# Kernel tuning notes

Measured on AMD Instinct MI355X. Metric: run time of the kernel, lower is better.

The kernel has to match this reference:

```python
import jax, jax.numpy as jnp
import numpy as np

H, DK, DV, CHUNK = 4, 256, 256, 32
MIN_FLOOR, MAX_FLOOR, TEMP_MIN = 0.01, 0.1, 0.5


def _silu(x):
    return x * jax.nn.sigmoid(x)


def _causal_dw_conv(x_bcl, w_ck):
    # depthwise causal 1-D conv: x (b, C, L), w (C, K)
    K = w_ck.shape[-1]
    return jax.lax.conv_general_dilated(
        x_bcl, w_ck[:, None, :], window_strides=(1,), padding=[(K - 1, 0)],
        feature_group_count=x_bcl.shape[1])


def _l2norm(x):
    return x * jax.lax.rsqrt(jnp.sum(x * x, axis=-1, keepdims=True) + 1e-6)


def _delta_rule_chunkwise(q, k, v, beta, chunk=CHUNK):
    # q,k: (b,h,L,dk)  v: (b,h,L,dv)  beta: (b,h,L); L divisible by chunk
    b, h, L, dk = q.shape
    dv = v.shape[-1]
    n = L // chunk
    q = _l2norm(q)
    k = _l2norm(k)
    v = v * beta[..., None]
    kb = k * beta[..., None]
    qc, kc, vc, kbc = (t.reshape(b, h, n, chunk, -1) for t in (q, k, v, kb))
    # in-chunk inverse: the torch row loop computes (I + tril(k_beta k^T, -1))^{-1}
    A = jnp.einsum('bhncd,bhned->bhnce', kbc, kc)
    eye = jnp.eye(chunk, dtype=q.dtype)
    T = eye + jnp.tril(A, -1)
    inv = jax.scipy.linalg.solve_triangular(
        T, jnp.broadcast_to(eye, T.shape), lower=True, unit_diagonal=True)
    u = inv @ vc      # (b,h,n,c,dv)
    w = inv @ kbc     # (b,h,n,c,dk)
    strict = jnp.triu(jnp.ones((chunk, chunk), dtype=bool), 1)

    def step(S, xs):
        q_i, k_i, u_i, w_i = xs
        att = jnp.where(strict, 0.0, jnp.einsum('bhcd,bhed->bhce', q_i, k_i))
        u_adj = u_i - jnp.einsum('bhck,bhkd->bhcd', w_i, S)
        o = jnp.einsum('bhck,bhkd->bhcd', q_i, S) + att @ u_adj
        S = S + jnp.einsum('bhck,bhcd->bhkd', k_i, u_adj)
        return S, o

    mv = lambda t: jnp.moveaxis(t, 2, 0)  # chunks to scan axis
    S0 = jnp.zeros((b, h, dk, dv), dtype=q.dtype)
    S, outs = jax.lax.scan(step, S0, (mv(qc), mv(kc), mv(u), mv(w)))
    out = jnp.moveaxis(outs, 0, 2).reshape(b, h, L, dv)
    return out, S


def _fir(x, filt):
    # x: (b,l,h,d), filt: (h,d,K) depthwise causal FIR per (head, channel)
    b, l, h, d = x.shape
    xc = x.transpose(0, 2, 3, 1).reshape(b, h * d, l)
    y = _causal_dw_conv(xc, filt.reshape(h * d, -1))
    return y.reshape(b, h, d, l).transpose(0, 3, 1, 2)


def setup_inputs() -> dict:
    key = jax.random.key(0)
    ks = iter(jax.random.split(key, 32))
    B, L, D = 4, 2048, 1024
    kd, vd = H * DK, H * DV
    rn = lambda shp, s=0.02: jax.random.normal(next(ks), shp, jnp.float32) * s
    fir = lambda K: (jnp.zeros((H, DV, K), jnp.float32).at[..., -1].set(1.0)
                     + 0.01 * jax.random.normal(next(ks), (H, DV, K), jnp.float32))
    return dict(
        hidden_states=jax.random.normal(next(ks), (B, L, D), jnp.float32),
        Wq=rn((D, kd)), Wk=rn((D, kd)), Wv=rn((D, vd)),
        q_conv_w=rn((kd, 4), 0.3), k_conv_w=rn((kd, 4), 0.3), v_conv_w=rn((vd, 4), 0.3),
        Wb=rn((D, H)),
        fir_w3=fir(3), fir_w7=fir(7), fir_w15=fir(15), fir_w31=fir(31),
        router_W1=rn((D + DV * H * 5, 2 * D)), router_b1=jnp.zeros((2 * D,), jnp.float32),
        router_W2=rn((2 * D, H * 5)), router_b2=jnp.zeros((H * 5,), jnp.float32),
        id_gate_W=rn((D, H)), id_gate_b=jnp.full((H,), 2.0, jnp.float32),
        log_tau=jnp.zeros((H,), jnp.float32),
        o_norm_w=jnp.ones((DV,), jnp.float32),
        Wo=rn((vd, D)))


def reference(hidden_states, Wq, Wk, Wv, q_conv_w, k_conv_w, v_conv_w, Wb,
              fir_w3, fir_w7, fir_w15, fir_w31,
              router_W1, router_b1, router_W2, router_b2,
              id_gate_W, id_gate_b, log_tau, o_norm_w, Wo):
    B, L, D = hidden_states.shape
    conv = lambda x, w: _silu(_causal_dw_conv(x.transpose(0, 2, 1), w)).transpose(0, 2, 1)
    q = conv(hidden_states @ Wq, q_conv_w).reshape(B, L, H, DK)
    k = conv(hidden_states @ Wk, k_conv_w).reshape(B, L, H, DK)
    v_direct = conv(hidden_states @ Wv, v_conv_w).reshape(B, L, H, DV)
    beta = jax.nn.sigmoid(hidden_states @ Wb)  # (B,L,H)
    delta_out, _ = _delta_rule_chunkwise(
        q.transpose(0, 2, 1, 3), k.transpose(0, 2, 1, 3),
        v_direct.transpose(0, 2, 1, 3), beta.transpose(0, 2, 1))
    delta_out = delta_out.transpose(0, 2, 1, 3)  # (B,L,H,DV)
    paths = [_fir(v_direct, f) for f in (fir_w3, fir_w7, fir_w15, fir_w31)] + [delta_out]
    # token-adaptive value/context split
    p_value = jax.nn.sigmoid(hidden_states @ id_gate_W + id_gate_b)  # (B,L,H)
    floor_tok = MIN_FLOOR + (MAX_FLOOR - MIN_FLOOR) * (1.0 - p_value)
    p_value_adj = (1.0 - floor_tok) * p_value
    context_mass = 1.0 - p_value_adj
    # router over [hidden, all context paths]
    router_in = jnp.concatenate(
        [hidden_states] + [p.reshape(B, L, H * DV) for p in paths], axis=-1)
    hmid = jax.nn.gelu(router_in @ router_W1 + router_b1, approximate=False)
    logits = (hmid @ router_W2 + router_b2).reshape(B, L, H, 5)
    tau = jnp.maximum(jnp.exp(log_tau), TEMP_MIN)  # (H,)
    probs = jax.nn.softmax(logits / tau[:, None], axis=-1)
    ctx = sum(probs[..., i:i + 1] * paths[i] for i in range(5))
    o = context_mass[..., None] * ctx + p_value_adj[..., None] * v_direct
    # per-head RMSNorm then output projection
    o = o * jax.lax.rsqrt(jnp.mean(o * o, axis=-1, keepdims=True) + 1e-5) * o_norm_w
    return o.reshape(B, L, H * DV) @ Wo
```

## Files before the change

### kernel.cpp

```cpp
#include <hip/hip_runtime.h>
#include <math.h>

#define NTOK   8192
#define LSEQ   2048
#define NCHUNK 64

typedef short bhalf8 __attribute__((ext_vector_type(8)));
typedef float floatx4 __attribute__((ext_vector_type(4)));

__device__ inline ushort f2bf(float f) {
  uint u = __float_as_uint(f);
  u += 0x7FFFu + ((u >> 16) & 1u);
  return (ushort)(u >> 16);
}
__device__ inline float bf2f(ushort h) {
  return __uint_as_float(((uint)h) << 16);
}

#define GLD_LDS16(g, s) __builtin_amdgcn_global_load_lds(                      \
    (const __attribute__((address_space(1))) void*)(g),                        \
    (__attribute__((address_space(3))) void*)(s), 16, 0, 0)

__global__ __launch_bounds__(256)
void cvt_bf16(const float* __restrict__ x, ushort* __restrict__ y, int n8) {
  int i = blockIdx.x * 256 + threadIdx.x;
  if (i >= n8) return;
  const float4* xp = (const float4*)x;
  float4 a = xp[2 * i], b = xp[2 * i + 1];
  uint4 o;
  o.x = (uint)f2bf(a.x) | ((uint)f2bf(a.y) << 16);
  o.y = (uint)f2bf(a.z) | ((uint)f2bf(a.w) << 16);
  o.z = (uint)f2bf(b.x) | ((uint)f2bf(b.y) << 16);
  o.w = (uint)f2bf(b.z) | ((uint)f2bf(b.w) << 16);
  ((uint4*)y)[i] = o;
}

__global__ __launch_bounds__(256)
void cvt_t(const float* __restrict__ x, ushort* __restrict__ y, int R, int C) {
  __shared__ float tile[32][33];
  int r0 = blockIdx.y * 32, c0 = blockIdx.x * 32;
  int tr = threadIdx.x >> 5;
  int tc = threadIdx.x & 31;
  #pragma unroll
  for (int rr = tr; rr < 32; rr += 8)
    tile[rr][tc] = x[(size_t)(r0 + rr) * C + c0 + tc];
  __syncthreads();
  #pragma unroll
  for (int rr = tr; rr < 32; rr += 8)
    y[(size_t)(c0 + rr) * R + r0 + tc] = f2bf(tile[tc][rr]);
}

template<int ACC>
__global__ __launch_bounds__(256)
void gemm_bf(const ushort* __restrict__ A, const ushort* __restrict__ BT,
             float* __restrict__ C, int K, int lda, int ldbt, int ldc) {
  __shared__ ushort Asm[128 * 32];
  __shared__ ushort Bsm[128 * 32];
  const int t = threadIdx.x;
  const int w = t >> 6, l = t & 63;
  const int m0 = blockIdx.y * 128, n0 = blockIdx.x * 128;
  const int wr = w >> 1, wc = w & 1;
  const int srow = l >> 2;
  const int scol = (l & 3) * 8;
  const int fr = l & 15;
  const int fk = (l >> 4) * 8;

  floatx4 acc[4][4];
  #pragma unroll
  for (int i = 0; i < 4; i++)
    #pragma unroll
    for (int j = 0; j < 4; j++)
      #pragma unroll
      for (int r = 0; r < 4; r++) acc[i][j][r] = 0.f;

  for (int k0 = 0; k0 < K; k0 += 32) {
    __syncthreads();
    #pragma unroll
    for (int j = 0; j < 2; j++) {
      int row = w * 32 + j * 16 + srow;
      GLD_LDS16(A + (size_t)(m0 + row) * lda + k0 + scol,
                Asm + (w * 32 + j * 16) * 32);
      GLD_LDS16(BT + (size_t)(n0 + row) * ldbt + k0 + scol,
                Bsm + (w * 32 + j * 16) * 32);
    }
    __syncthreads();
    bhalf8 af[4], bf_[4];
    #pragma unroll
    for (int i = 0; i < 4; i++)
      af[i] = *(const bhalf8*)&Asm[(wr * 64 + i * 16 + fr) * 32 + fk];
    #pragma unroll
    for (int j = 0; j < 4; j++)
      bf_[j] = *(const bhalf8*)&Bsm[(wc * 64 + j * 16 + fr) * 32 + fk];
    #pragma unroll
    for (int i = 0; i < 4; i++)
      #pragma unroll
      for (int j = 0; j < 4; j++)
        acc[i][j] = __builtin_amdgcn_mfma_f32_16x16x32_bf16(af[i], bf_[j],
                                                            acc[i][j], 0, 0, 0);
  }
  const int crow = (l >> 4) * 4;
  const int ccol = l & 15;
  #pragma unroll
  for (int i = 0; i < 4; i++)
    #pragma unroll
    for (int j = 0; j < 4; j++) {
      float* cp = &C[(size_t)(m0 + wr * 64 + i * 16 + crow) * ldc +
                     n0 + wc * 64 + j * 16 + ccol];
      #pragma unroll
      for (int r = 0; r < 4; r++) {
        if (ACC) cp[(size_t)r * ldc] += acc[i][j][r];
        else     cp[(size_t)r * ldc]  = acc[i][j][r];
      }
    }
}

struct APtrs { const ushort* p[6]; };

__global__ __launch_bounds__(256)
void gemm_router(APtrs ap, const ushort* __restrict__ BT,
                 float* __restrict__ C) {
  __shared__ ushort Asm[128 * 32];
  __shared__ ushort Bsm[128 * 32];
  const int t = threadIdx.x;
  const int w = t >> 6, l = t & 63;
  const int m0 = blockIdx.y * 128, n0 = blockIdx.x * 128;
  const int wr = w >> 1, wc = w & 1;
  const int srow = l >> 2;
  const int scol = (l & 3) * 8;
  const int fr = l & 15;
  const int fk = (l >> 4) * 8;

  floatx4 acc[4][4];
  #pragma unroll
  for (int i = 0; i < 4; i++)
    #pragma unroll
    for (int j = 0; j < 4; j++)
      #pragma unroll
      for (int r = 0; r < 4; r++) acc[i][j][r] = 0.f;

  for (int k0 = 0; k0 < 6144; k0 += 32) {
    const ushort* Abase = ap.p[k0 >> 10];
    const int kk = k0 & 1023;
    __syncthreads();
    #pragma unroll
    for (int j = 0; j < 2; j++) {
      int row = w * 32 + j * 16 + srow;
      GLD_LDS16(Abase + (size_t)(m0 + row) * 1024 + kk + scol,
                Asm + (w * 32 + j * 16) * 32);
      GLD_LDS16(BT + (size_t)(n0 + row) * 6144 + k0 + scol,
                Bsm + (w * 32 + j * 16) * 32);
    }
    __syncthreads();
    bhalf8 af[4], bf_[4];
    #pragma unroll
    for (int i = 0; i < 4; i++)
      af[i] = *(const bhalf8*)&Asm[(wr * 64 + i * 16 + fr) * 32 + fk];
    #pragma unroll
    for (int j = 0; j < 4; j++)
      bf_[j] = *(const bhalf8*)&Bsm[(wc * 64 + j * 16 + fr) * 32 + fk];
    #pragma unroll
    for (int i = 0; i < 4; i++)
      #pragma unroll
      for (int j = 0; j < 4; j++)
        acc[i][j] = __builtin_amdgcn_mfma_f32_16x16x32_bf16(af[i], bf_[j],
                                                            acc[i][j], 0, 0, 0);
  }
  const int crow = (l >> 4) * 4;
  const int ccol = l & 15;
  #pragma unroll
  for (int i = 0; i < 4; i++)
    #pragma unroll
    for (int j = 0; j < 4; j++) {
      float* cp = &C[(size_t)(m0 + wr * 64 + i * 16 + crow) * 1024 +
                     n0 + wc * 64 + j * 16 + ccol];
      #pragma unroll
      for (int r = 0; r < 4; r++) cp[(size_t)r * 1024] = acc[i][j][r];
    }
}

__global__ __launch_bounds__(256)
void conv4_silu(const float* __restrict__ x, const float* __restrict__ w,
                float* __restrict__ y) {
  int idx = blockIdx.x * 256 + threadIdx.x;
  int c = idx & 1023;
  int bl = idx >> 10;
  int l = bl & (LSEQ - 1);
  float w0 = w[c * 4 + 0], w1 = w[c * 4 + 1], w2 = w[c * 4 + 2], w3 = w[c * 4 + 3];
  float acc = x[idx] * w3;
  if (l >= 1) acc += x[idx - 1024] * w2;
  if (l >= 2) acc += x[idx - 2048] * w1;
  if (l >= 3) acc += x[idx - 3072] * w0;
  y[idx] = acc / (1.f + expf(-acc));
}

__global__ __launch_bounds__(256)
void pack_fir(const float* __restrict__ f3w, const float* __restrict__ f7w,
              const float* __restrict__ f15w, const float* __restrict__ f31w,
              float* __restrict__ fwTp) {
  int i = blockIdx.x * 256 + threadIdx.x;
  if (i >= 57344) return;
  int row = i >> 10, c = i & 1023;
  float val;
  if (row < 3)       val = f3w[c * 3 + row];
  else if (row < 10) val = f7w[c * 7 + (row - 3)];
  else if (row < 25) val = f15w[c * 15 + (row - 10)];
  else               val = f31w[c * 31 + (row - 25)];
  fwTp[i] = val;
}

__global__ __launch_bounds__(256)
void fir_all(const float* __restrict__ v, const float* __restrict__ fwTp,
             ushort* __restrict__ y3, ushort* __restrict__ y7,
             ushort* __restrict__ y15, ushort* __restrict__ y31) {
  int idx = blockIdx.x * 256 + threadIdx.x;
  int c = idx & 1023;
  int l = (idx >> 10) & (LSEQ - 1);
  float a3 = 0.f, a7 = 0.f, a15 = 0.f, a31 = 0.f;
  #pragma unroll
  for (int back = 30; back >= 0; back--) {
    float x = (l >= back) ? v[idx - back * 1024] : 0.f;
    a31 += x * fwTp[(25 + 30 - back) * 1024 + c];
    if (back <= 14) a15 += x * fwTp[(10 + 14 - back) * 1024 + c];
    if (back <= 6)  a7  += x * fwTp[(3 + 6 - back) * 1024 + c];
    if (back <= 2)  a3  += x * fwTp[(2 - back) * 1024 + c];
  }
  y3[idx]  = f2bf(a3);
  y7[idx]  = f2bf(a7);
  y15[idx] = f2bf(a15);
  y31[idx] = f2bf(a31);
}

__global__ __launch_bounds__(256)
void beta_pv(const float* __restrict__ hs, const float* __restrict__ Wb,
             const float* __restrict__ idW, const float* __restrict__ idb,
             float* __restrict__ beta, float* __restrict__ pv) {
  int tok = blockIdx.x;
  int h = threadIdx.x >> 6;
  int lane = threadIdx.x & 63;
  const float* hrow = hs + (size_t)tok * 1024;
  float s1 = 0.f, s2 = 0.f;
  #pragma unroll
  for (int j = 0; j < 16; j++) {
    int d = lane + j * 64;
    float hv = hrow[d];
    s1 += hv * Wb[d * 4 + h];
    s2 += hv * idW[d * 4 + h];
  }
  #pragma unroll
  for (int off = 32; off; off >>= 1) {
    s1 += __shfl_down(s1, off);
    s2 += __shfl_down(s2, off);
  }
  if (lane == 0) {
    beta[tok * 4 + h] = 1.f / (1.f + expf(-s1));
    pv[tok * 4 + h] = 1.f / (1.f + expf(-(s2 + idb[h])));
  }
}

__global__ __launch_bounds__(256)
void l2norm_qk(float* __restrict__ q, float* __restrict__ k) {
  int tok = blockIdx.x;
  int h = threadIdx.x >> 6;
  int lane = threadIdx.x & 63;
  size_t base = (size_t)tok * 1024 + h * 256 + lane * 4;
  {
    float4* p = (float4*)(q + base);
    float4 v = *p;
    float ss = v.x * v.x + v.y * v.y + v.z * v.z + v.w * v.w;
    #pragma unroll
    for (int off = 32; off; off >>= 1) ss += __shfl_xor(ss, off);
    float sc = rsqrtf(ss + 1e-6f);
    v.x *= sc; v.y *= sc; v.z *= sc; v.w *= sc;
    *p = v;
  }
  {
    float4* p = (float4*)(k + base);
    float4 v = *p;
    float ss = v.x * v.x + v.y * v.y + v.z * v.z + v.w * v.w;
    #pragma unroll
    for (int off = 32; off; off >>= 1) ss += __shfl_xor(ss, off);
    float sc = rsqrtf(ss + 1e-6f);
    v.x *= sc; v.y *= sc; v.z *= sc; v.w *= sc;
    *p = v;
  }
}

__global__ __launch_bounds__(256)
void chunk_prep(const float* __restrict__ q, const float* __restrict__ k,
                const float* __restrict__ v, const float* __restrict__ beta,
                ushort* __restrict__ attf, float* __restrict__ ub,
                ushort* __restrict__ wfb, ushort* __restrict__ qfb,
                ushort* __restrict__ ktb) {
  __shared__ float kbuf[32 * 260];
  __shared__ float qbuf[32 * 260];
  __shared__ float Am[32 * 32];
  __shared__ float bet[32];
  const int t = threadIdx.x;
  const int blk = blockIdx.x;
  const int n = blk & 63, bh = blk >> 6;
  const int h = bh & 3, b = bh >> 2;
  const size_t rowbase = (size_t)b * LSEQ + n * 32;
  const int cbase = h * 256;
  const int srow = t >> 6, scol = (t & 63) * 4;
  const size_t fb = (size_t)blk * 8192;

  #pragma unroll
  for (int rep = 0; rep < 8; rep++) {
    int r = rep * 4 + srow;
    *(float4*)&kbuf[r * 260 + scol] =
        *(const float4*)&k[(rowbase + r) * 1024 + cbase + scol];
    *(float4*)&qbuf[r * 260 + scol] =
        *(const float4*)&q[(rowbase + r) * 1024 + cbase + scol];
  }
  if (t < 32) bet[t] = beta[(rowbase + t) * 4 + h];
  __syncthreads();

  #pragma unroll
  for (int e = 0; e < 4; e++) {
    int idx = t + e * 256;
    int i = idx >> 5, jc = idx & 31;
    float da = 0.f, dq = 0.f;
    for (int d0 = 0; d0 < 256; d0 += 4) {
      float4 kj = *(float4*)&kbuf[jc * 260 + d0];
      float4 ki = *(float4*)&kbuf[i * 260 + d0];
      float4 qi = *(float4*)&qbuf[i * 260 + d0];
      da += ki.x * kj.x + ki.y * kj.y + ki.z * kj.z + ki.w * kj.w;
      dq += qi.x * kj.x + qi.y * kj.y + qi.z * kj.z + qi.w * kj.w;
    }
    Am[i * 32 + jc] = (jc < i) ? bet[i] * da : 0.f;
    float av = (jc <= i) ? dq : 0.f;
    attf[(size_t)blk * 1024 + (i >> 4) * 512 +
         ((i & 15) + ((jc >> 3) & 3) * 16) * 8 + (jc & 7)] = f2bf(av);
  }
  __syncthreads();

  #pragma unroll
  for (int cg = 0; cg < 4; cg++) {
    bhalf8 pk;
    #pragma unroll
    for (int j = 0; j < 8; j++)
      pk[j] = (short)f2bf(kbuf[(cg * 8 + j) * 260 + t]);
    *(bhalf8*)&ktb[fb + (t >> 4) * 512 + ((t & 15) + cg * 16) * 8] = pk;
  }

  #pragma unroll 1
  for (int i = 0; i < 32; i++) {
    float val = bet[i] * kbuf[i * 260 + t];
    for (int j = 0; j < i; j++) val -= Am[i * 32 + j] * kbuf[j * 260 + t];
    kbuf[i * 260 + t] = val;
  }
  __syncthreads();

  #pragma unroll
  for (int rep = 0; rep < 4; rep++) {
    int p = rep * 256 + t;
    int c = p & 31, dk8 = p >> 5;
    size_t pos = fb + ((size_t)(dk8 >> 2) * 2 + (c >> 4)) * 512 +
                 ((c & 15) + (dk8 & 3) * 16) * 8;
    bhalf8 pw, pq;
    #pragma unroll
    for (int j = 0; j < 8; j++) {
      pw[j] = (short)f2bf(kbuf[c * 260 + dk8 * 8 + j]);
      pq[j] = (short)f2bf(qbuf[c * 260 + dk8 * 8 + j]);
    }
    *(bhalf8*)&wfb[pos] = pw;
    *(bhalf8*)&qfb[pos] = pq;
  }
  __syncthreads();

  #pragma unroll
  for (int rep = 0; rep < 8; rep++) {
    int r = rep * 4 + srow;
    *(float4*)&qbuf[r * 260 + scol] =
        *(const float4*)&v[(rowbase + r) * 1024 + cbase + scol];
  }
  __syncthreads();
  #pragma unroll 1
  for (int i = 0; i < 32; i++) {
    float val = bet[i] * qbuf[i * 260 + t];
    for (int j = 0; j < i; j++) val -= Am[i * 32 + j] * qbuf[j * 260 + t];
    qbuf[i * 260 + t] = val;
  }
  for (int j = 0; j < 32; j++)
    ub[(rowbase + j) * 1024 + cbase + t] = qbuf[j * 260 + t];
}

__global__ __launch_bounds__(256)
void delta_scan(const ushort* __restrict__ wfb, const ushort* __restrict__ qfb,
                const ushort* __restrict__ ktb, const ushort* __restrict__ attf,
                const float* __restrict__ ub, ushort* __restrict__ outb) {
  __shared__ ushort wS[8192];
  __shared__ ushort qS[8192];
  __shared__ ushort kTS[8192];
  __shared__ ushort attS[1024];
  __shared__ ushort SbT[16 * 264];
  __shared__ ushort uaT[16 * 40];
  __shared__ float pbufW[4 * 544];
  __shared__ float pbufQ[4 * 544];
  __shared__ float oacc[544];
  const int t = threadIdx.x;
  const int w = t >> 6, l = t & 63;
  const int col16 = l & 15, g = l >> 4;
  const int blk = blockIdx.x;
  const int dsl = blk & 15, bh = blk >> 4;
  const int h = bh & 3, b = bh >> 2;
  const int dbase = h * 256 + dsl * 16;

  floatx4 S_acc[4];
  #pragma unroll
  for (int m = 0; m < 4; m++)
    #pragma unroll
    for (int r = 0; r < 4; r++) S_acc[m][r] = 0.f;

  for (int n = 0; n < NCHUNK; n++) {
    const size_t cb = ((size_t)(bh * 64 + n)) * 8192;
    const size_t ab = ((size_t)(bh * 64 + n)) * 1024;
    const size_t rowbase = (size_t)b * LSEQ + n * 32;

    #pragma unroll
    for (int m = 0; m < 4; m++) {
      uint lo = (uint)f2bf(S_acc[m][0]) | ((uint)f2bf(S_acc[m][1]) << 16);
      uint hi = (uint)f2bf(S_acc[m][2]) | ((uint)f2bf(S_acc[m][3]) << 16);
      uint2 pk; pk.x = lo; pk.y = hi;
      *(uint2*)&SbT[col16 * 264 + w * 64 + m * 16 + g * 4] = pk;
    }
    #pragma unroll
    for (int i = 0; i < 4; i++) {
      GLD_LDS16(wfb + cb + (w * 4 + i) * 512 + l * 8, &wS[(w * 4 + i) * 512]);
      GLD_LDS16(qfb + cb + (w * 4 + i) * 512 + l * 8, &qS[(w * 4 + i) * 512]);
      GLD_LDS16(ktb + cb + (w * 4 + i) * 512 + l * 8, &kTS[(w * 4 + i) * 512]);
    }
    if (w == 2) {
      GLD_LDS16(attf + ab + l * 8, &attS[0]);
      GLD_LDS16(attf + ab + 512 + l * 8, &attS[512]);
    }
    float u0 = ub[(rowbase + (t >> 4)) * 1024 + dbase + (t & 15)];
    float u1 = ub[(rowbase + 16 + (t >> 4)) * 1024 + dbase + (t & 15)];
    __syncthreads();

    floatx4 pw0, pw1, pq0, pq1;
    #pragma unroll
    for (int r = 0; r < 4; r++) { pw0[r] = 0.f; pw1[r] = 0.f; pq0[r] = 0.f; pq1[r] = 0.f; }
    #pragma unroll
    for (int s = 0; s < 2; s++) {
      const int koff = w * 2 + s;
      bhalf8 sb = *(const bhalf8*)&SbT[col16 * 264 + koff * 32 + g * 8];
      bhalf8 wa0 = *(const bhalf8*)&wS[((koff * 2 + 0) * 64 + l) * 8];
      bhalf8 wa1 = *(const bhalf8*)&wS[((koff * 2 + 1) * 64 + l) * 8];
      bhalf8 qa0 = *(const bhalf8*)&qS[((koff * 2 + 0) * 64 + l) * 8];
      bhalf8 qa1 = *(const bhalf8*)&qS[((koff * 2 + 1) * 64 + l) * 8];
      pw0 = __builtin_amdgcn_mfma_f32_16x16x32_bf16(wa0, sb, pw0, 0, 0, 0);
      pw1 = __builtin_amdgcn_mfma_f32_16x16x32_bf16(wa1, sb, pw1, 0, 0, 0);
      pq0 = __builtin_amdgcn_mfma_f32_16x16x32_bf16(qa0, sb, pq0, 0, 0, 0);
      pq1 = __builtin_amdgcn_mfma_f32_16x16x32_bf16(qa1, sb, pq1, 0, 0, 0);
    }
    #pragma unroll
    for (int r = 0; r < 4; r++) {
      pbufW[w * 544 + (g * 4 + r) * 17 + col16] = pw0[r];
      pbufW[w * 544 + (16 + g * 4 + r) * 17 + col16] = pw1[r];
      pbufQ[w * 544 + (g * 4 + r) * 17 + col16] = pq0[r];
      pbufQ[w * 544 + (16 + g * 4 + r) * 17 + col16] = pq1[r];
    }
    __syncthreads();

    {
      const int row = t >> 4, c2 = t & 15;
      const int i0 = row * 17 + c2, i1 = (row + 16) * 17 + c2;
      float wsA = pbufW[i0] + pbufW[544 + i0] + pbufW[1088 + i0] + pbufW[1632 + i0];
      float wsB = pbufW[i1] + pbufW[544 + i1] + pbufW[1088 + i1] + pbufW[1632 + i1];
      float qsA = pbufQ[i0] + pbufQ[544 + i0] + pbufQ[1088 + i0] + pbufQ[1632 + i0];
      float qsB = pbufQ[i1] + pbufQ[544 + i1] + pbufQ[1088 + i1] + pbufQ[1632 + i1];
      oacc[i0] = qsA;
      oacc[i1] = qsB;
      uaT[c2 * 40 + row] = f2bf(u0 - wsA);
      uaT[c2 * 40 + row + 16] = f2bf(u1 - wsB);
    }
    __syncthreads();

    bhalf8 uB = *(const bhalf8*)&uaT[col16 * 40 + g * 8];
    #pragma unroll
    for (int m = 0; m < 4; m++) {
      bhalf8 ka = *(const bhalf8*)&kTS[((w * 4 + m) * 64 + l) * 8];
      S_acc[m] = __builtin_amdgcn_mfma_f32_16x16x32_bf16(ka, uB, S_acc[m], 0, 0, 0);
    }
    if (w < 2) {
      floatx4 z;
      #pragma unroll
      for (int r = 0; r < 4; r++) z[r] = 0.f;
      bhalf8 aa = *(const bhalf8*)&attS[(w * 64 + l) * 8];
      floatx4 oat = __builtin_amdgcn_mfma_f32_16x16x32_bf16(aa, uB, z, 0, 0, 0);
      #pragma unroll
      for (int r = 0; r < 4; r++) {
        int row = w * 16 + g * 4 + r;
        float ov = oacc[row * 17 + col16] + oat[r];
        outb[(rowbase + row) * 1024 + dbase + col16] = f2bf(ov);
      }
    }
    __syncthreads();
  }
}

__global__ __launch_bounds__(256)
void gelu_bias(float* __restrict__ x, const float* __restrict__ bias) {
  int idx = blockIdx.x * 256 + threadIdx.x;
  float4* p = (float4*)x + idx;
  float4 v = *p;
  int col = (idx * 4) & 1023;
  float4 bb = *(const float4*)&bias[col];
  float xs[4] = {v.x + bb.x, v.y + bb.y, v.z + bb.z, v.w + bb.w};
  #pragma unroll
  for (int j = 0; j < 4; j++)
    xs[j] = 0.5f * xs[j] * (1.f + erff(xs[j] * 0.70710678118654752f));
  v.x = xs[0]; v.y = xs[1]; v.z = xs[2]; v.w = xs[3];
  *p = v;
}

template<int FIRST>
__global__ __launch_bounds__(256)
void logits_acc(const float* __restrict__ hmid, const float* __restrict__ W2,
                const float* __restrict__ b2, float* __restrict__ logits) {
  __shared__ float hrow[1024];
  __shared__ float part[8][20];
  int tok = blockIdx.x, t = threadIdx.x;
  ((float4*)hrow)[t] = ((const float4*)(hmid + (size_t)tok * 1024))[t];
  __syncthreads();
  if (t < 160) {
    int col = t % 20, seg = t / 20;
    float acc = 0.f;
    for (int kk = 0; kk < 128; kk++) {
      int k2 = seg * 128 + kk;
      acc += hrow[k2] * W2[(size_t)k2 * 20 + col];
    }
    part[seg][col] = acc;
  }
  __syncthreads();
  if (t < 20) {
    float s = 0.f;
    #pragma unroll
    for (int g = 0; g < 8; g++) s += part[g][t];
    if (FIRST) logits[(size_t)tok * 20 + t] = b2[t] + s;
    else       logits[(size_t)tok * 20 + t] += s;
  }
}

__global__ __launch_bounds__(256)
void softmax_probs(const float* __restrict__ logits, const float* __restrict__ ltau,
                   float* __restrict__ probs) {
  int idx = blockIdx.x * 256 + threadIdx.x;
  int tok = idx >> 2, h = idx & 3;
  float tau = expf(ltau[h]);
  tau = tau < 0.5f ? 0.5f : tau;
  float x[5]; float m = -1e30f;
  #pragma unroll
  for (int i = 0; i < 5; i++) {
    x[i] = logits[(size_t)tok * 20 + h * 5 + i] / tau;
    m = fmaxf(m, x[i]);
  }
  float s = 0.f;
  #pragma unroll
  for (int i = 0; i < 5; i++) { x[i] = expf(x[i] - m); s += x[i]; }
  float inv = 1.f / s;
  #pragma unroll
  for (int i = 0; i < 5; i++) probs[(size_t)tok * 20 + h * 5 + i] = x[i] * inv;
}

__global__ __launch_bounds__(256)
void mix_rms(const ushort* __restrict__ f3, const ushort* __restrict__ f7,
             const ushort* __restrict__ f15, const ushort* __restrict__ f31,
             const ushort* __restrict__ dlt, const float* __restrict__ v,
             const float* __restrict__ probs, const float* __restrict__ pv,
             const float* __restrict__ onw, ushort* __restrict__ omix) {
  int tok = blockIdx.x;
  int h = threadIdx.x >> 6;
  int lane = threadIdx.x & 63;
  size_t base = (size_t)tok * 1024 + h * 256 + lane * 4;
  const float* pp = probs + (size_t)tok * 20 + h * 5;
  float p0 = pp[0], p1 = pp[1], p2 = pp[2], p3 = pp[3], p4 = pp[4];
  float pvv = pv[tok * 4 + h];
  float floor_tok = 0.01f + 0.09f * (1.f - pvv);
  float pa = (1.f - floor_tok) * pvv;
  float cm = 1.f - pa;
  ushort4 a4 = *(const ushort4*)&f3[base];
  ushort4 b4 = *(const ushort4*)&f7[base];
  ushort4 c4 = *(const ushort4*)&f15[base];
  ushort4 d4 = *(const ushort4*)&f31[base];
  ushort4 e4 = *(const ushort4*)&dlt[base];
  float4 vv = *(const float4*)&v[base];
  float av[4] = {bf2f(a4.x), bf2f(a4.y), bf2f(a4.z), bf2f(a4.w)};
  float bv[4] = {bf2f(b4.x), bf2f(b4.y), bf2f(b4.z), bf2f(b4.w)};
  float cv[4] = {bf2f(c4.x), bf2f(c4.y), bf2f(c4.z), bf2f(c4.w)};
  float dv[4] = {bf2f(d4.x), bf2f(d4.y), bf2f(d4.z), bf2f(d4.w)};
  float ev[4] = {bf2f(e4.x), bf2f(e4.y), bf2f(e4.z), bf2f(e4.w)};
  float vvv[4] = {vv.x, vv.y, vv.z, vv.w};
  float o[4];
  #pragma unroll
  for (int j = 0; j < 4; j++)
    o[j] = cm * (p0 * av[j] + p1 * bv[j] + p2 * cv[j] + p3 * dv[j] + p4 * ev[j]) +
           pa * vvv[j];
  float ss = o[0]*o[0] + o[1]*o[1] + o[2]*o[2] + o[3]*o[3];
  #pragma unroll
  for (int off = 32; off; off >>= 1) ss += __shfl_xor(ss, off);
  float sc = rsqrtf(ss * (1.f / 256.f) + 1e-5f);
  float4 wn = *(const float4*)&onw[lane * 4];
  ushort4 res;
  res.x = f2bf(o[0] * sc * wn.x); res.y = f2bf(o[1] * sc * wn.y);
  res.z = f2bf(o[2] * sc * wn.z); res.w = f2bf(o[3] * sc * wn.w);
  *(ushort4*)&omix[base] = res;
}

extern "C" void kernel_launch(void* const* d_in, const int* in_sizes, int n_in,
                              void* d_out, int out_size, void* d_ws, size_t ws_size,
                              hipStream_t stream) {
  const float* hs  = (const float*)d_in[0];
  const float* Wq  = (const float*)d_in[1];
  const float* Wk  = (const float*)d_in[2];
  const float* Wv  = (const float*)d_in[3];
  const float* qcw = (const float*)d_in[4];
  const float* kcw = (const float*)d_in[5];
  const float* vcw = (const float*)d_in[6];
  const float* Wb  = (const float*)d_in[7];
  const float* f3w = (const float*)d_in[8];
  const float* f7w = (const float*)d_in[9];
  const float* f15w= (const float*)d_in[10];
  const float* f31w= (const float*)d_in[11];
  const float* rW1 = (const float*)d_in[12];
  const float* rb1 = (const float*)d_in[13];
  const float* rW2 = (const float*)d_in[14];
  const float* rb2 = (const float*)d_in[15];
  const float* igW = (const float*)d_in[16];
  const float* igb = (const float*)d_in[17];
  const float* ltau= (const float*)d_in[18];
  const float* onw = (const float*)d_in[19];
  const float* Wo  = (const float*)d_in[20];
  float* out = (float*)d_out;
  float* ws  = (float*)d_ws;

  float* pre    = ws;
  float* qb     = ws +  8388608;
  float* kb     = ws + 16777216;
  float* vb     = ws + 25165824;
  float* ub     = ws + 33554432;
  float* wbuf   = ws + 41943040;
  float* dlt    = ws + 50331648;
  float* fwTp   = ws + 58720256;
  float* beta   = ws + 59768832;
  float* pv     = ws + 59801600;
  float* logits = ws + 59834368;
  float* probs  = ws + 59998208;

  ushort* hs_bf1 = (ushort*)ub;
  ushort* WqT    = (ushort*)(ub + 4194304);
  ushort* WkT    = WqT + 1048576;
  ushort* WvT    = WkT + 1048576;
  ushort* ktb    = (ushort*)pre;
  ushort* attfb  = (ushort*)(pre + 4194304);
  ushort* wfb    = (ushort*)wbuf;
  ushort* qfb    = (ushort*)(wbuf + 4194304);
  ushort* f3b    = (ushort*)ub;
  ushort* f7b    = (ushort*)(ub + 4194304);
  ushort* f15b   = (ushort*)wbuf;
  ushort* f31b   = (ushort*)(wbuf + 4194304);
  ushort* dltb   = (ushort*)dlt;
  ushort* omixb  = (ushort*)(dlt + 4194304);
  ushort* hs_bf2 = (ushort*)kb;
  ushort* WoT    = (ushort*)(kb + 4194304);
  ushort* W1T    = (ushort*)qb;
  float*  hmid   = pre;

  dim3 blk(256);
  dim3 gg(8, 64);

  cvt_bf16<<<4096, blk, 0, stream>>>(hs, hs_bf1, 1048576);
  cvt_t<<<dim3(32, 32), blk, 0, stream>>>(Wq, WqT, 1024, 1024);
  cvt_t<<<dim3(32, 32), blk, 0, stream>>>(Wk, WkT, 1024, 1024);
  cvt_t<<<dim3(32, 32), blk, 0, stream>>>(Wv, WvT, 1024, 1024);
  gemm_bf<0><<<gg, blk, 0, stream>>>(hs_bf1, WqT, pre, 1024, 1024, 1024, 1024);
  conv4_silu<<<32768, blk, 0, stream>>>(pre, qcw, qb);
  gemm_bf<0><<<gg, blk, 0, stream>>>(hs_bf1, WkT, pre, 1024, 1024, 1024, 1024);
  conv4_silu<<<32768, blk, 0, stream>>>(pre, kcw, kb);
  gemm_bf<0><<<gg, blk, 0, stream>>>(hs_bf1, WvT, pre, 1024, 1024, 1024, 1024);
  conv4_silu<<<32768, blk, 0, stream>>>(pre, vcw, vb);

  beta_pv<<<8192, blk, 0, stream>>>(hs, Wb, igW, igb, beta, pv);
  l2norm_qk<<<8192, blk, 0, stream>>>(qb, kb);

  chunk_prep<<<1024, blk, 0, stream>>>(qb, kb, vb, beta, attfb, ub, wfb, qfb, ktb);
  delta_scan<<<256, blk, 0, stream>>>(wfb, qfb, ktb, attfb, ub, dltb);

  pack_fir<<<224, blk, 0, stream>>>(f3w, f7w, f15w, f31w, fwTp);
  fir_all<<<32768, blk, 0, stream>>>(vb, fwTp, f3b, f7b, f15b, f31b);

  cvt_bf16<<<4096, blk, 0, stream>>>(hs, hs_bf2, 1048576);
  cvt_t<<<dim3(64, 192), blk, 0, stream>>>(rW1, W1T, 6144, 2048);
  cvt_t<<<dim3(32, 32), blk, 0, stream>>>(Wo, WoT, 1024, 1024);

  APtrs ap;
  ap.p[0] = hs_bf2; ap.p[1] = f3b; ap.p[2] = f7b;
  ap.p[3] = f15b;   ap.p[4] = f31b; ap.p[5] = dltb;
  for (int nh = 0; nh < 2; nh++) {
    gemm_router<<<gg, blk, 0, stream>>>(ap, W1T + (size_t)nh * 1024 * 6144, hmid);
    gelu_bias<<<8192, blk, 0, stream>>>(hmid, rb1 + nh * 1024);
    if (nh == 0) logits_acc<1><<<8192, blk, 0, stream>>>(hmid, rW2, rb2, logits);
    else         logits_acc<0><<<8192, blk, 0, stream>>>(hmid, rW2 + (size_t)1024 * 20, rb2, logits);
  }
  softmax_probs<<<128, blk, 0, stream>>>(logits, ltau, probs);

  mix_rms<<<8192, blk, 0, stream>>>(f3b, f7b, f15b, f31b, dltb, vb, probs, pv,
                                    onw, omixb);
  gemm_bf<0><<<gg, blk, 0, stream>>>(omixb, WoT, out, 1024, 1024, 1024, 1024);
}
```

Baseline: 1.247 ms.

## Store GEMM tiles in MFMA fragment order and fuse bias+GELU into router GEMM

Changes the LDS staging layout of both GEMM kernels so each 16-row subtile is written in the exact lane order the MFMA fragment reads, making fragment loads contiguous and removing LDS bank conflicts. Also fuses the router's first-layer bias add and exact GELU into the router GEMM epilogue, eliminating the standalone gelu_bias kernel and its read/write pass over the hidden buffer. The epilogue now does erff per output element inside the GEMM, adding some register and ALU pressure there.

```diff
diff --git a/kernel.cpp b/kernel.cpp
--- a/kernel.cpp
+++ b/kernel.cpp
@@ -60,10 +60,8 @@
   const int w = t >> 6, l = t & 63;
   const int m0 = blockIdx.y * 128, n0 = blockIdx.x * 128;
   const int wr = w >> 1, wc = w & 1;
-  const int srow = l >> 2;
-  const int scol = (l & 3) * 8;
-  const int fr = l & 15;
-  const int fk = (l >> 4) * 8;
+  const int frow = l & 15;
+  const int fcol = (l >> 4) * 8;
 
   floatx4 acc[4][4];
   #pragma unroll
@@ -77,20 +75,19 @@
     __syncthreads();
     #pragma unroll
     for (int j = 0; j < 2; j++) {
-      int row = w * 32 + j * 16 + srow;
-      GLD_LDS16(A + (size_t)(m0 + row) * lda + k0 + scol,
-                Asm + (w * 32 + j * 16) * 32);
-      GLD_LDS16(BT + (size_t)(n0 + row) * ldbt + k0 + scol,
-                Bsm + (w * 32 + j * 16) * 32);
+      int sub = w * 2 + j;
+      int row = sub * 16 + frow;
+      GLD_LDS16(A + (size_t)(m0 + row) * lda + k0 + fcol, Asm + sub * 512);
+      GLD_LDS16(BT + (size_t)(n0 + row) * ldbt + k0 + fcol, Bsm + sub * 512);
     }
     __syncthreads();
     bhalf8 af[4], bf_[4];
     #pragma unroll
     for (int i = 0; i < 4; i++)
-      af[i] = *(const bhalf8*)&Asm[(wr * 64 + i * 16 + fr) * 32 + fk];
+      af[i] = *(const bhalf8*)&Asm[(wr * 4 + i) * 512 + l * 8];
     #pragma unroll
     for (int j = 0; j < 4; j++)
-      bf_[j] = *(const bhalf8*)&Bsm[(wc * 64 + j * 16 + fr) * 32 + fk];
+      bf_[j] = *(const bhalf8*)&Bsm[(wc * 4 + j) * 512 + l * 8];
     #pragma unroll
     for (int i = 0; i < 4; i++)
       #pragma unroll
@@ -118,17 +115,15 @@
 
 __global__ __launch_bounds__(256)
 void gemm_router(APtrs ap, const ushort* __restrict__ BT,
-                 float* __restrict__ C) {
+                 const float* __restrict__ bias, float* __restrict__ C) {
   __shared__ ushort Asm[128 * 32];
   __shared__ ushort Bsm[128 * 32];
   const int t = threadIdx.x;
   const int w = t >> 6, l = t & 63;
   const int m0 = blockIdx.y * 128, n0 = blockIdx.x * 128;
   const int wr = w >> 1, wc = w & 1;
-  const int srow = l >> 2;
-  const int scol = (l & 3) * 8;
-  const int fr = l & 15;
-  const int fk = (l >> 4) * 8;
+  const int frow = l & 15;
+  const int fcol = (l >> 4) * 8;
 
   floatx4 acc[4][4];
   #pragma unroll
@@ -144,20 +139,19 @@
     __syncthreads();
     #pragma unroll
     for (int j = 0; j < 2; j++) {
-      int row = w * 32 + j * 16 + srow;
-      GLD_LDS16(Abase + (size_t)(m0 + row) * 1024 + kk + scol,
-                Asm + (w * 32 + j * 16) * 32);
-      GLD_LDS16(BT + (size_t)(n0 + row) * 6144 + k0 + scol,
-                Bsm + (w * 32 + j * 16) * 32);
+      int sub = w * 2 + j;
+      int row = sub * 16 + frow;
+      GLD_LDS16(Abase + (size_t)(m0 + row) * 1024 + kk + fcol, Asm + sub * 512);
+      GLD_LDS16(BT + (size_t)(n0 + row) * 6144 + k0 + fcol, Bsm + sub * 512);
     }
     __syncthreads();
     bhalf8 af[4], bf_[4];
     #pragma unroll
     for (int i = 0; i < 4; i++)
-      af[i] = *(const bhalf8*)&Asm[(wr * 64 + i * 16 + fr) * 32 + fk];
+      af[i] = *(const bhalf8*)&Asm[(wr * 4 + i) * 512 + l * 8];
     #pragma unroll
     for (int j = 0; j < 4; j++)
-      bf_[j] = *(const bhalf8*)&Bsm[(wc * 64 + j * 16 + fr) * 32 + fk];
+      bf_[j] = *(const bhalf8*)&Bsm[(wc * 4 + j) * 512 + l * 8];
     #pragma unroll
     for (int i = 0; i < 4; i++)
       #pragma unroll
@@ -171,10 +165,14 @@
   for (int i = 0; i < 4; i++)
     #pragma unroll
     for (int j = 0; j < 4; j++) {
-      float* cp = &C[(size_t)(m0 + wr * 64 + i * 16 + crow) * 1024 +
-                     n0 + wc * 64 + j * 16 + ccol];
-      #pragma unroll
-      for (int r = 0; r < 4; r++) cp[(size_t)r * 1024] = acc[i][j][r];
+      const int col = n0 + wc * 64 + j * 16 + ccol;
+      const float bb = bias[col];
+      float* cp = &C[(size_t)(m0 + wr * 64 + i * 16 + crow) * 1024 + col];
+      #pragma unroll
+      for (int r = 0; r < 4; r++) {
+        float x = acc[i][j][r] + bb;
+        cp[(size_t)r * 1024] = 0.5f * x * (1.f + erff(x * 0.70710678118654752f));
+      }
     }
 }
 
@@ -498,21 +496,6 @@
     }
     __syncthreads();
   }
-}
-
-__global__ __launch_bounds__(256)
-void gelu_bias(float* __restrict__ x, const float* __restrict__ bias) {
-  int idx = blockIdx.x * 256 + threadIdx.x;
-  float4* p = (float4*)x + idx;
-  float4 v = *p;
-  int col = (idx * 4) & 1023;
-  float4 bb = *(const float4*)&bias[col];
-  float xs[4] = {v.x + bb.x, v.y + bb.y, v.z + bb.z, v.w + bb.w};
-  #pragma unroll
-  for (int j = 0; j < 4; j++)
-    xs[j] = 0.5f * xs[j] * (1.f + erff(xs[j] * 0.70710678118654752f));
-  v.x = xs[0]; v.y = xs[1]; v.z = xs[2]; v.w = xs[3];
-  *p = v;
 }
 
 template<int FIRST>
@@ -698,8 +681,8 @@
   ap.p[0] = hs_bf2; ap.p[1] = f3b; ap.p[2] = f7b;
   ap.p[3] = f15b;   ap.p[4] = f31b; ap.p[5] = dltb;
   for (int nh = 0; nh < 2; nh++) {
-    gemm_router<<<gg, blk, 0, stream>>>(ap, W1T + (size_t)nh * 1024 * 6144, hmid);
-    gelu_bias<<<8192, blk, 0, stream>>>(hmid, rb1 + nh * 1024);
+    gemm_router<<<gg, blk, 0, stream>>>(ap, W1T + (size_t)nh * 1024 * 6144,
+                                        rb1 + nh * 1024, hmid);
     if (nh == 0) logits_acc<1><<<8192, blk, 0, stream>>>(hmid, rW2, rb2, logits);
     else         logits_acc<0><<<8192, blk, 0, stream>>>(hmid, rW2 + (size_t)1024 * 20, rb2, logits);
   }
```

Result: slower. 1.351 ms (+8.4%).
